# Optimization experiments

Measured on AMD Instinct MI355X. Metric: run time of the kernel, lower is better.

The kernel has to match this reference:

```python
import jax, jax.numpy as jnp
import numpy as np

HQ, HKV, D, RD = 32, 8, 128, 64   # q heads, kv heads, head_dim, rotary_dim
EPS = 1e-6


def _rms_norm(x, w, eps):
    # per-head RMSNorm over last dim (non-gemma: scale by w)
    var = jnp.mean(x * x, axis=-1, keepdims=True)
    return x * jax.lax.rsqrt(var + eps) * w


def _partial_rope(x, c, s, rd):
    # x: [T, H, D]; c/s: [T, rd//2]; NeoX half-split rotation on first rd dims
    x1 = x[..., : rd // 2]
    x2 = x[..., rd // 2 : rd]
    c = c[:, None, :]
    s = s[:, None, :]
    return jnp.concatenate([x1 * c - x2 * s, x2 * c + x1 * s, x[..., rd:]], axis=-1)


def setup_inputs() -> dict:
    key = jax.random.key(0)
    ks = jax.random.split(key, 6)
    B, QL, HID, CACHE = 4, 512, 4096, 512
    T = B * QL
    MAXPOS = 4096
    NPAGES, PS, MP = 256, 16, 64  # total pages, page_size, max pages per seq

    hidden_states = jax.random.normal(ks[0], (T, HID), jnp.float32)
    inv = 1.0 / (10000.0 ** (np.arange(0, RD, 2, dtype=np.float64) / RD))
    ang = np.arange(MAXPOS)[:, None] * inv[None, :]
    cos = jnp.asarray(np.cos(ang), jnp.float32)   # [MAXPOS, RD//2]
    sin = jnp.asarray(np.sin(ang), jnp.float32)
    positions = jnp.tile(CACHE + jnp.arange(QL, dtype=jnp.int32), B)  # [T]
    k_cache = jax.random.normal(ks[1], (NPAGES, PS, HKV, D), jnp.float32)
    v_cache = jax.random.normal(ks[2], (NPAGES, PS, HKV, D), jnp.float32)
    page_table = jnp.arange(B * MP, dtype=jnp.int32).reshape(B, MP)
    cache_seqlens = jnp.full((B,), CACHE, jnp.int32)
    cu_seqlens_q = jnp.arange(B + 1, dtype=jnp.int32) * QL
    qkv_weight = jax.random.normal(ks[3], ((HQ + 2 * HKV) * D, HID), jnp.float32) * 0.02
    o_proj_weight = jax.random.normal(ks[4], (HID, HQ * D), jnp.float32) * 0.02
    q_norm_weight = jnp.ones((D,), jnp.float32)
    k_norm_weight = jnp.ones((D,), jnp.float32)
    return dict(hidden_states=hidden_states, cos=cos, sin=sin, positions=positions,
                k_cache=k_cache, v_cache=v_cache, page_table=page_table,
                cache_seqlens=cache_seqlens, cu_seqlens_q=cu_seqlens_q,
                qkv_weight=qkv_weight, o_proj_weight=o_proj_weight,
                q_norm_weight=q_norm_weight, k_norm_weight=k_norm_weight)


def reference(hidden_states, cos, sin, positions, k_cache, v_cache, page_table,
              cache_seqlens, cu_seqlens_q, qkv_weight, o_proj_weight,
              q_norm_weight, k_norm_weight):
    T = hidden_states.shape[0]
    B = cache_seqlens.shape[0]
    QL = T // B                       # equal-length sequences (extend mode)
    PS = k_cache.shape[1]

    # QKV projection + split
    qkv = hidden_states @ qkv_weight.T
    q, k, v = jnp.split(qkv, [HQ * D, (HQ + HKV) * D], axis=-1)

    # per-head QK RMSNorm (q_norm_weight.shape[0] == head_dim branch)
    q = _rms_norm(q.reshape(T, HQ, D), q_norm_weight, EPS)
    k = _rms_norm(k.reshape(T, HKV, D), k_norm_weight, EPS)
    v = v.reshape(T, HKV, D)

    # partial RoPE
    pc, psn = cos[positions], sin[positions]
    q = _partial_rope(q, pc, psn, RD)
    k = _partial_rope(k, pc, psn, RD)

    # paged KV-cache write: absolute slot = cache_seqlens[b] + j
    pos_abs = cache_seqlens[:, None] + jnp.arange(QL, dtype=jnp.int32)[None, :]  # [B,QL]
    pages = jnp.take_along_axis(page_table, pos_abs // PS, axis=1)
    slots = pos_abs % PS
    k_cache = k_cache.at[pages, slots].set(k.reshape(B, QL, HKV, D))
    v_cache = v_cache.at[pages, slots].set(v.reshape(B, QL, HKV, D))

    # gather per-sequence KV from pages: [B, KV, HKV, D]
    KV = page_table.shape[1] * PS
    keys = k_cache[page_table].reshape(B, KV, HKV, D)
    vals = v_cache[page_table].reshape(B, KV, HKV, D)

    # GQA paged attention with causal mask on absolute positions
    G = HQ // HKV
    qh = q.reshape(B, QL, HKV, G, D)
    scale = 1.0 / np.sqrt(D).astype(np.float32)
    scores = jnp.einsum('bqhgd,bkhd->bhgqk', qh, keys) * scale
    kpos = jnp.arange(KV, dtype=jnp.int32)
    mask = kpos[None, None, :] <= pos_abs[:, :, None]                  # [B,QL,KV]
    scores = jnp.where(mask[:, None, None, :, :], scores, -1e30)
    probs = jax.nn.softmax(scores, axis=-1)
    attn = jnp.einsum('bhgqk,bkhd->bqhgd', probs, vals).reshape(T, HQ * D)

    return attn @ o_proj_weight.T
```

## Files before the change

### kernel.cpp

```cpp
#include <hip/hip_runtime.h>

typedef unsigned int   u32;
typedef unsigned short u16;

typedef float  f32x4  __attribute__((ext_vector_type(4)));
typedef u32    u32x4  __attribute__((ext_vector_type(4)));
typedef u16    u16x4  __attribute__((ext_vector_type(4)));
typedef __bf16 bf16x8 __attribute__((ext_vector_type(8)));

union FragU { u16 us[8]; u32x4 q; bf16x8 v; };

__device__ __forceinline__ u32 f2u(float x){ union{float f;u32 u;}c; c.f=x; return c.u; }
__device__ __forceinline__ float u2f(u32 u){ union{float f;u32 u;}c; c.u=u; return c.f; }
__device__ __forceinline__ u16 bfhi(float x){ u32 u=f2u(x); return (u16)((u + 0x7fffu + ((u>>16)&1u))>>16); }
__device__ __forceinline__ u32 cvtpk(float a, float b){
  u32 r;
  asm("v_cvt_pk_bf16_f32 %0, %1, %2" : "=v"(r) : "v"(a), "v"(b));
  return r;
}

__device__ __forceinline__ void gload16(const void* g, void* l){
  __builtin_amdgcn_global_load_lds(
      (const __attribute__((address_space(1))) unsigned int*)g,
      (__attribute__((address_space(3))) unsigned int*)l, 16, 0, 0);
}

__global__ __launch_bounds__(256)
void prep_pack(const float* __restrict__ s0, u32* __restrict__ d0,
               const float* __restrict__ s1, u32* __restrict__ d1,
               const float* __restrict__ s2, u32* __restrict__ d2)
{
  const int bid = blockIdx.x;
  const float* s; u32* d; int base;
  if (bid < 256)       { s = s0; d = d0; base = bid*4096; }
  else if (bid < 1024) { s = s1; d = d1; base = (bid-256)*4096; }
  else                 { s = s2; d = d2; base = (bid-1024)*4096; }
  int j = base + threadIdx.x;
  #pragma unroll
  for (int it=0; it<8; ++it){
    const int j2 = j + 256;
    f32x4 a0 = __builtin_nontemporal_load(reinterpret_cast<const f32x4*>(s) + 2*j);
    f32x4 a1 = __builtin_nontemporal_load(reinterpret_cast<const f32x4*>(s) + 2*j + 1);
    f32x4 b0 = __builtin_nontemporal_load(reinterpret_cast<const f32x4*>(s) + 2*j2);
    f32x4 b1 = __builtin_nontemporal_load(reinterpret_cast<const f32x4*>(s) + 2*j2 + 1);
    reinterpret_cast<u32x4*>(d)[j] =
      (u32x4){ cvtpk(a0.x,a0.y), cvtpk(a0.z,a0.w), cvtpk(a1.x,a1.y), cvtpk(a1.z,a1.w) };
    reinterpret_cast<u32x4*>(d)[j2] =
      (u32x4){ cvtpk(b0.x,b0.y), cvtpk(b0.z,b0.w), cvtpk(b1.x,b1.y), cvtpk(b1.z,b1.w) };
    j += 512;
  }
}

__global__ __launch_bounds__(256, 2)
void gemm_pkA2(const u16* __restrict__ A, const u16* __restrict__ B,
               float* __restrict__ C, int M, int N, int K)
{
  extern __shared__ char smem[];
  const int tid  = threadIdx.x;
  const int lane = tid & 63;
  const int w    = tid >> 6;
  const int wm = w >> 1, wn = w & 1;
  const int ln = lane & 15, lg = lane >> 4;

  const int nbm = M >> 7;
  const int nbn = N / 192;
  const int nwg = nbm * nbn;
  const int swz = (blockIdx.x & 7) * (nwg >> 3) + (blockIdx.x >> 3);
  const int bm = swz % nbm, bn = swz / nbm;

  const size_t rb = (size_t)K * 2;
  const int lrow  = lane >> 3;
  const int lslot = (lane & 7) ^ (lrow & 7);
  const char* As0 = (const char*)A + (size_t)(bm*128 + w*8 + lrow)*rb + lslot*16;
  const char* Bs0 = (const char*)B + (size_t)(bn*192 + w*8 + lrow)*rb + lslot*16;

  auto stA = [&](int buf, int t) {
    const char* s = As0 + ((size_t)t << 7);
    char* d = smem + buf*40960 + w*1024;
    gload16(s,           d);
    gload16(s +  32*rb,  d + 4096);
    gload16(s +  64*rb,  d + 8192);
    gload16(s +  96*rb,  d + 12288);
  };
  auto stB = [&](int buf, int t) {
    const char* s = Bs0 + ((size_t)t << 7);
    char* d = smem + buf*40960 + 16384 + w*1024;
    gload16(s,           d);
    gload16(s +  32*rb,  d + 4096);
    gload16(s +  64*rb,  d + 8192);
    gload16(s +  96*rb,  d + 12288);
    gload16(s + 128*rb,  d + 16384);
    gload16(s + 160*rb,  d + 20480);
  };

  f32x4 z = {0.f,0.f,0.f,0.f};
  f32x4 acc[4][6];
  #pragma unroll
  for (int i=0;i<4;i++){
    #pragma unroll
    for (int j=0;j<6;j++) acc[i][j] = z;
  }

  const int nt = K >> 6;
  stA(0, 0); stB(0, 0);
  if (nt > 1) { stB(1, 1);
    asm volatile("s_waitcnt vmcnt(6)" ::: "memory");
  } else {
    asm volatile("s_waitcnt vmcnt(0)" ::: "memory");
  }
  __builtin_amdgcn_s_barrier();
  asm volatile("" ::: "memory");

  const int lx7 = ln & 7;

  for (int t = 0; t < nt; ++t){
    const int cur = t & 1;
    const char* bufc = smem + cur*40960;

    FragU bfr[6][2];
    #pragma unroll
    for (int ni=0; ni<6; ni++){
      const int rofs = 16384 + (wn*96 + ni*16 + ln)*128;
      #pragma unroll
      for (int ks=0; ks<2; ks++)
        bfr[ni][ks].q = *reinterpret_cast<const u32x4*>(bufc + rofs + (((ks*4+lg)^lx7)<<4));
    }
    FragU af[2][2];
    #pragma unroll
    for (int mf=0; mf<2; mf++){
      const int rofs = (wm*64 + mf*16 + ln)*128;
      #pragma unroll
      for (int ks=0; ks<2; ks++)
        af[mf][ks].q = *reinterpret_cast<const u32x4*>(bufc + rofs + (((ks*4+lg)^lx7)<<4));
    }
    if (t+1 < nt) stA(cur^1, t+1);
    __builtin_amdgcn_s_barrier();
    __builtin_amdgcn_s_setprio(1);
    #pragma unroll
    for (int ks=0; ks<2; ks++){
      #pragma unroll
      for (int mf=0; mf<2; mf++){
        #pragma unroll
        for (int ni=0; ni<6; ni++)
          acc[mf][ni] = __builtin_amdgcn_mfma_f32_16x16x32_bf16(af[mf][ks].v, bfr[ni][ks].v, acc[mf][ni], 0,0,0);
      }
    }
    __builtin_amdgcn_s_setprio(0);
    asm volatile("s_waitcnt lgkmcnt(0)" ::: "memory");
    __builtin_amdgcn_s_barrier();

    FragU ag[2][2];
    #pragma unroll
    for (int mf=0; mf<2; mf++){
      const int rofs = (wm*64 + (mf+2)*16 + ln)*128;
      #pragma unroll
      for (int ks=0; ks<2; ks++)
        ag[mf][ks].q = *reinterpret_cast<const u32x4*>(bufc + rofs + (((ks*4+lg)^lx7)<<4));
    }
    if (t+2 < nt) stB(cur, t+2);
    __builtin_amdgcn_s_barrier();
    __builtin_amdgcn_s_setprio(1);
    #pragma unroll
    for (int ks=0; ks<2; ks++){
      #pragma unroll
      for (int mf=0; mf<2; mf++){
        #pragma unroll
        for (int ni=0; ni<6; ni++)
          acc[mf+2][ni] = __builtin_amdgcn_mfma_f32_16x16x32_bf16(ag[mf][ks].v, bfr[ni][ks].v, acc[mf+2][ni], 0,0,0);
      }
    }
    __builtin_amdgcn_s_setprio(0);
    if (t+1 < nt){
      if (t+2 < nt) asm volatile("s_waitcnt vmcnt(6)" ::: "memory");
      else          asm volatile("s_waitcnt vmcnt(0)" ::: "memory");
    }
    __builtin_amdgcn_s_barrier();
    asm volatile("" ::: "memory");
  }

  #pragma unroll
  for (int mi=0; mi<4; mi++){
    #pragma unroll
    for (int ni=0; ni<6; ni++){
      const int row0 = bm*128 + wm*64 + mi*16 + lg*4;
      const int col  = bn*192 + wn*96 + ni*16 + ln;
      #pragma unroll
      for (int r=0; r<4; r++)
        C[(size_t)(row0+r)*N + col] = acc[mi][ni][r];
    }
  }
}

__global__ __launch_bounds__(256, 2)
void gemm_pkB2(const u16* __restrict__ A, const u16* __restrict__ B,
               float* __restrict__ C, int M, int N, int K)
{
  extern __shared__ char smem[];
  const int tid  = threadIdx.x;
  const int lane = tid & 63;
  const int w    = tid >> 6;
  const int wm = w >> 1, wn = w & 1;
  const int ln = lane & 15, lg = lane >> 4;

  const int nbm = M >> 7, nbn = N >> 7;
  const int nwg = nbm * nbn;
  const int swz = (blockIdx.x & 7) * (nwg >> 3) + (blockIdx.x >> 3);
  const int bm = swz % nbm, bn = swz / nbm;

  const size_t rb = (size_t)K * 2;
  const int lrow  = lane >> 3;
  const int lslot = (lane & 7) ^ (lrow & 7);
  const char* As0 = (const char*)A + (size_t)(bm*128 + w*8 + lrow)*rb + lslot*16;
  const char* Bs0 = (const char*)B + (size_t)(bn*128 + w*8 + lrow)*rb + lslot*16;

  auto stA = [&](int buf, int t) {
    const char* s = As0 + ((size_t)t << 7);
    char* d = smem + buf*32768 + w*1024;
    gload16(s,           d);
    gload16(s +  32*rb,  d + 4096);
    gload16(s +  64*rb,  d + 8192);
    gload16(s +  96*rb,  d + 12288);
  };
  auto stB = [&](int buf, int t) {
    const char* s = Bs0 + ((size_t)t << 7);
    char* d = smem + buf*32768 + 16384 + w*1024;
    gload16(s,           d);
    gload16(s +  32*rb,  d + 4096);
    gload16(s +  64*rb,  d + 8192);
    gload16(s +  96*rb,  d + 12288);
  };

  f32x4 z = {0.f,0.f,0.f,0.f};
  f32x4 acc[4][4];
  #pragma unroll
  for (int i=0;i<4;i++){
    #pragma unroll
    for (int j=0;j<4;j++) acc[i][j] = z;
  }

  const int nt = K >> 6;
  stA(0, 0); stB(0, 0);
  if (nt > 1) { stB(1, 1);
    asm volatile("s_waitcnt vmcnt(4)" ::: "memory");
  } else {
    asm volatile("s_waitcnt vmcnt(0)" ::: "memory");
  }
  __builtin_amdgcn_s_barrier();
  asm volatile("" ::: "memory");

  const int lx7 = ln & 7;

  for (int t = 0; t < nt; ++t){
    const int cur = t & 1;
    const char* bufc = smem + cur*32768;

    FragU bfr[4][2];
    #pragma unroll
    for (int ni=0; ni<4; ni++){
      const int rofs = 16384 + (wn*64 + ni*16 + ln)*128;
      #pragma unroll
      for (int ks=0; ks<2; ks++)
        bfr[ni][ks].q = *reinterpret_cast<const u32x4*>(bufc + rofs + (((ks*4+lg)^lx7)<<4));
    }
    FragU af[2][2];
    #pragma unroll
    for (int mf=0; mf<2; mf++){
      const int rofs = (wm*64 + mf*16 + ln)*128;
      #pragma unroll
      for (int ks=0; ks<2; ks++)
        af[mf][ks].q = *reinterpret_cast<const u32x4*>(bufc + rofs + (((ks*4+lg)^lx7)<<4));
    }
    if (t+1 < nt) stA(cur^1, t+1);
    __builtin_amdgcn_s_barrier();
    __builtin_amdgcn_s_setprio(1);
    #pragma unroll
    for (int ks=0; ks<2; ks++){
      #pragma unroll
      for (int mf=0; mf<2; mf++){
        #pragma unroll
        for (int ni=0; ni<4; ni++)
          acc[mf][ni] = __builtin_amdgcn_mfma_f32_16x16x32_bf16(af[mf][ks].v, bfr[ni][ks].v, acc[mf][ni], 0,0,0);
      }
    }
    __builtin_amdgcn_s_setprio(0);
    asm volatile("s_waitcnt lgkmcnt(0)" ::: "memory");
    __builtin_amdgcn_s_barrier();

    FragU ag[2][2];
    #pragma unroll
    for (int mf=0; mf<2; mf++){
      const int rofs = (wm*64 + (mf+2)*16 + ln)*128;
      #pragma unroll
      for (int ks=0; ks<2; ks++)
        ag[mf][ks].q = *reinterpret_cast<const u32x4*>(bufc + rofs + (((ks*4+lg)^lx7)<<4));
    }
    if (t+2 < nt) stB(cur, t+2);
    __builtin_amdgcn_s_barrier();
    __builtin_amdgcn_s_setprio(1);
    #pragma unroll
    for (int ks=0; ks<2; ks++){
      #pragma unroll
      for (int mf=0; mf<2; mf++){
        #pragma unroll
        for (int ni=0; ni<4; ni++)
          acc[mf+2][ni] = __builtin_amdgcn_mfma_f32_16x16x32_bf16(ag[mf][ks].v, bfr[ni][ks].v, acc[mf+2][ni], 0,0,0);
      }
    }
    __builtin_amdgcn_s_setprio(0);
    if (t+1 < nt){
      if (t+2 < nt) asm volatile("s_waitcnt vmcnt(4)" ::: "memory");
      else          asm volatile("s_waitcnt vmcnt(0)" ::: "memory");
    }
    __builtin_amdgcn_s_barrier();
    asm volatile("" ::: "memory");
  }

  #pragma unroll
  for (int mi=0; mi<4; mi++){
    #pragma unroll
    for (int ni=0; ni<4; ni++){
      const int row0 = bm*128 + wm*64 + mi*16 + lg*4;
      const int col  = bn*128 + wn*64 + ni*16 + ln;
      #pragma unroll
      for (int r=0; r<4; r++)
        C[(size_t)(row0+r)*N + col] = acc[mi][ni][r];
    }
  }
}

__global__ __launch_bounds__(256)
void norm_gather_kv(const float* __restrict__ qkv, const float* __restrict__ cosT,
                    const float* __restrict__ sinT, const int* __restrict__ positions,
                    const int* __restrict__ cache_seqlens,
                    const float* __restrict__ kw,
                    const float* __restrict__ k_cache, const float* __restrict__ v_cache,
                    const int* __restrict__ page_table,
                    u16* __restrict__ k_all, u16* __restrict__ v_allT)
{
  const int tid = threadIdx.x;
  if (blockIdx.x < 2048){
    const int t = blockIdx.x;
    const int lane = tid & 63;
    const int w = tid >> 6;
    const int b = t >> 9;
    const int q = t & 511;
    const int pos  = positions[t];
    const int cpos = cache_seqlens[b] + q;
    for (int it=0; it<4; ++it){
      int hh = it*4 + w;
      const float* xp = qkv + (size_t)t*6144 + (32+hh)*128 + 2*lane;
      float2 x = *reinterpret_cast<const float2*>(xp);
      if (hh < 8){
        float ss = x.x*x.x + x.y*x.y;
        #pragma unroll
        for (int mk=1; mk<64; mk<<=1) ss += __shfl_xor(ss, mk);
        float var = ss*(1.0f/128.0f) + 1e-6f;
        float rq = rsqrtf(var);
        rq = rq*(1.5f - 0.5f*var*rq*rq);
        x.x *= rq*kw[2*lane]; x.y *= rq*kw[2*lane+1];
        float px = __shfl_xor(x.x, 16);
        float py = __shfl_xor(x.y, 16);
        if (lane < 32){
          int ci = pos*32 + 2*(lane&15);
          float2 cc = *reinterpret_cast<const float2*>(cosT + ci);
          float2 sc = *reinterpret_cast<const float2*>(sinT + ci);
          if (lane < 16){ x.x = x.x*cc.x - px*sc.x; x.y = x.y*cc.y - py*sc.y; }
          else          { x.x = x.x*cc.x + px*sc.x; x.y = x.y*cc.y + py*sc.y; }
        }
        u16* kp = k_all + ((size_t)(b*8 + hh)*1024 + cpos)*128 + 2*lane;
        kp[0] = bfhi(x.x); kp[1] = bfhi(x.y);
      } else {
        u16* vp = v_allT + ((size_t)(b*8 + (hh-8))*128 + 2*lane)*1024 + cpos;
        vp[0]    = bfhi(x.x);
        vp[1024] = bfhi(x.y);
      }
    }
    return;
  }
  __shared__ float tb[32][129];
  const int id = blockIdx.x - 2048;
  const int jt = id & 31, h = (id>>5)&7, b = id>>8;
  const int j0 = jt*32;
  const int csb = cache_seqlens[b];
  if (j0 >= csb) return;
  {
    int r = tid>>3, c = tid&7;
    int j = j0 + r;
    int page = page_table[b*64 + (j>>4)];
    int slot = j & 15;
    const float* ks = k_cache + (size_t)((page*16 + slot)*8 + h)*128;
    const float* vs = v_cache + (size_t)((page*16 + slot)*8 + h)*128;
    u16* kd = k_all + ((size_t)(b*8+h)*1024 + j)*128;
    const bool wr = (j < csb);
    #pragma unroll
    for (int i=0;i<2;i++){
      int d0i = (c + 8*i)*8;
      f32x4 ka = __builtin_nontemporal_load(reinterpret_cast<const f32x4*>(ks + d0i));
      f32x4 kb = __builtin_nontemporal_load(reinterpret_cast<const f32x4*>(ks + d0i + 4));
      if (wr)
        *reinterpret_cast<u32x4*>(kd + d0i) =
          (u32x4){ cvtpk(ka.x,ka.y), cvtpk(ka.z,ka.w), cvtpk(kb.x,kb.y), cvtpk(kb.z,kb.w) };
      f32x4 va = __builtin_nontemporal_load(reinterpret_cast<const f32x4*>(vs + d0i));
      f32x4 vb = __builtin_nontemporal_load(reinterpret_cast<const f32x4*>(vs + d0i + 4));
      tb[r][d0i+0]=va.x; tb[r][d0i+1]=va.y; tb[r][d0i+2]=va.z; tb[r][d0i+3]=va.w;
      tb[r][d0i+4]=vb.x; tb[r][d0i+5]=vb.y; tb[r][d0i+6]=vb.z; tb[r][d0i+7]=vb.w;
    }
  }
  __syncthreads();
  {
    int dout = tid>>1, jh = tid&1;
    u16* vd = v_allT + ((size_t)(b*8+h)*128 + dout)*1024 + j0 + jh*16;
    #pragma unroll
    for (int i=0;i<2;i++){
      if (j0 + jh*16 + i*8 < csb){
        int jb = jh*16 + i*8;
        u32x4 o = { cvtpk(tb[jb+0][dout], tb[jb+1][dout]),
                    cvtpk(tb[jb+2][dout], tb[jb+3][dout]),
                    cvtpk(tb[jb+4][dout], tb[jb+5][dout]),
                    cvtpk(tb[jb+6][dout], tb[jb+7][dout]) };
        *reinterpret_cast<u32x4*>(vd + i*8) = o;
      }
    }
  }
}

__global__ __launch_bounds__(512)
void attn_fused9(const float* __restrict__ qkv, const float* __restrict__ cosT,
                 const float* __restrict__ sinT, const int* __restrict__ positions,
                 const float* __restrict__ qw,
                 const u16* __restrict__ k_all, const u16* __restrict__ v_allT,
                 const int* __restrict__ cache_seqlens, u16* __restrict__ attnO)
{
  extern __shared__ char smem[];
  const int tid = threadIdx.x, lane = tid&63, w = tid>>6;
  const int ln = lane&15, lg = lane>>4;
  const int id = blockIdx.x;
  const int qt = id & 3, g = (id>>2)&3, kvh = (id>>4)&7, b = id>>7;
  const int cs = cache_seqlens[b];
  const int h  = kvh*4 + g;
  const int q0 = qt*128 + w*16;
  const float SCALE = 0.08838834764831845f;
  f32x4 z = {0.f,0.f,0.f,0.f};

  FragU qf[4];
  {
    const int row = b*512 + q0 + ln;
    const float* qp = qkv + (size_t)row*6144 + h*128;
    float xq[4][8];
    float ss = 0.f;
    #pragma unroll
    for (int ks=0; ks<4; ks++){
      int d0 = ks*32 + lg*8;
      f32x4 a = *reinterpret_cast<const f32x4*>(qp + d0);
      f32x4 c = *reinterpret_cast<const f32x4*>(qp + d0 + 4);
      xq[ks][0]=a.x; xq[ks][1]=a.y; xq[ks][2]=a.z; xq[ks][3]=a.w;
      xq[ks][4]=c.x; xq[ks][5]=c.y; xq[ks][6]=c.z; xq[ks][7]=c.w;
      #pragma unroll
      for (int k2=0;k2<8;k2++) ss += xq[ks][k2]*xq[ks][k2];
    }
    ss += __shfl_xor(ss, 16);
    ss += __shfl_xor(ss, 32);
    float var = ss*(1.0f/128.0f) + 1e-6f;
    float rq = rsqrtf(var);
    rq = rq*(1.5f - 0.5f*var*rq*rq);
    rq *= SCALE;
    #pragma unroll
    for (int ks=0; ks<4; ks++){
      int d0 = ks*32 + lg*8;
      f32x4 wa = *reinterpret_cast<const f32x4*>(qw + d0);
      f32x4 wb = *reinterpret_cast<const f32x4*>(qw + d0 + 4);
      xq[ks][0]*=rq*wa.x; xq[ks][1]*=rq*wa.y; xq[ks][2]*=rq*wa.z; xq[ks][3]*=rq*wa.w;
      xq[ks][4]*=rq*wb.x; xq[ks][5]*=rq*wb.y; xq[ks][6]*=rq*wb.z; xq[ks][7]*=rq*wb.w;
    }
    const int pos = positions[row];
    const int ci = pos*32 + lg*8;
    #pragma unroll
    for (int k2=0;k2<8;k2+=4){
      f32x4 cc = *reinterpret_cast<const f32x4*>(cosT + ci + k2);
      f32x4 sc = *reinterpret_cast<const f32x4*>(sinT + ci + k2);
      float cA[4] = {cc.x,cc.y,cc.z,cc.w};
      float sA[4] = {sc.x,sc.y,sc.z,sc.w};
      #pragma unroll
      for (int u=0;u<4;u++){
        float x1 = xq[0][k2+u], x2 = xq[1][k2+u];
        xq[0][k2+u] = x1*cA[u] - x2*sA[u];
        xq[1][k2+u] = x2*cA[u] + x1*sA[u];
      }
    }
    #pragma unroll
    for (int ks=0; ks<4; ks++)
      qf[ks].q = (u32x4){ cvtpk(xq[ks][0],xq[ks][1]), cvtpk(xq[ks][2],xq[ks][3]),
                          cvtpk(xq[ks][4],xq[ks][5]), cvtpk(xq[ks][6],xq[ks][7]) };
  }

  f32x4 O[8];
  #pragma unroll
  for (int i=0;i<8;i++) O[i] = z;
  float lacc[4] = {0.f,0.f,0.f,0.f};
  const int prow0 = cs + q0 + lg*4;
  const int nt = (cs + qt*128 + 128 + 63) >> 6;
  const char* kbase = (const char*)(k_all  + (size_t)(b*8+kvh)*1024*128);
  const char* vbase = (const char*)(v_allT + (size_t)(b*8+kvh)*128*1024);

  auto stK = [&](int buf, int t){
    #pragma unroll
    for (int i=0;i<2;i++){
      int row = i*32 + w*4 + (lane>>4);
      const char* s = kbase + (size_t)(t*64 + row)*256 + (((lane&15) ^ (row&7))<<4);
      gload16(s, smem + buf*16384 + i*8192 + w*1024);
    }
  };
  auto stV = [&](int buf, int t){
    #pragma unroll
    for (int i=0;i<2;i++){
      int row = i*64 + w*8 + (lane>>3);
      const char* s = vbase + (size_t)row*2048 + (size_t)t*128 + (((lane&7) ^ (row&7))<<4);
      gload16(s, smem + 32768 + buf*16384 + i*8192 + w*1024);
    }
  };

  stK(0, 0); stV(0, 0);
  if (nt > 1){ stK(1, 1); stV(1, 1); }

  for (int tile=0; tile<nt; ++tile){
    const int cur = tile & 1;
    const int kv0 = tile*64;
    if (tile+1 < nt) asm volatile("s_waitcnt vmcnt(4)" ::: "memory");
    else             asm volatile("s_waitcnt vmcnt(0)" ::: "memory");
    __builtin_amdgcn_s_barrier();

    const u16* Kc = (const u16*)(smem + cur*16384);
    f32x4 s[4]; s[0]=z; s[1]=z; s[2]=z; s[3]=z;
    #pragma unroll
    for (int ks=0; ks<4; ks++){
      int so = ((ks*4+lg) ^ (ln&7)) << 3;
      #pragma unroll
      for (int n=0; n<4; n++){
        FragU kf;
        kf.q = *reinterpret_cast<const u32x4*>(&Kc[(n*16+ln)*128 + so]);
        s[n] = __builtin_amdgcn_mfma_f32_16x16x32_bf16(qf[ks].v, kf.v, s[n], 0,0,0);
      }
    }

    float pv[4][4];
    if (kv0 + 63 <= cs + q0){
      #pragma unroll
      for (int n=0;n<4;n++){
        #pragma unroll
        for (int r=0;r<4;r++) pv[n][r] = __expf(s[n][r]);
      }
    } else {
      #pragma unroll
      for (int n=0;n<4;n++){
        #pragma unroll
        for (int r=0;r<4;r++){
          bool ok = (kv0 + n*16 + ln) <= (prow0 + r);
          pv[n][r] = ok ? __expf(s[n][r]) : 0.f;
        }
      }
    }
    #pragma unroll
    for (int r=0;r<4;r++) lacc[r] += (pv[0][r] + pv[1][r]) + (pv[2][r] + pv[3][r]);

    #pragma unroll
    for (int n=0;n<4;n++){
      #pragma unroll
      for (int rp=0; rp<2; rp++){
        u32 hpk = cvtpk(pv[n][rp*2], pv[n][rp*2+1]);
        int col  = n*16 + ln;
        int row0 = lg*4 + rp*2;
        int b0 = w*2048 + row0*128 + ((((col>>3) ^ ((row0>>1)&7)))<<4) + (col&7)*2;
        *(u16*)(smem + 65536 + b0)       = (u16)hpk;
        *(u16*)(smem + 65536 + b0 + 128) = (u16)(hpk >> 16);
      }
    }
    FragU pa[2];
    #pragma unroll
    for (int ks2=0; ks2<2; ks2++)
      pa[ks2].q = *reinterpret_cast<const u32x4*>(
          smem + 65536 + w*2048 + ln*128 + (((ks2*4+lg) ^ ((ln>>1)&7))<<4));

    const char* Vb = smem + 32768 + cur*16384;
    #pragma unroll
    for (int nf=0; nf<8; nf++){
      int dr = nf*16 + ln;
      #pragma unroll
      for (int ks2=0; ks2<2; ks2++){
        FragU vf;
        vf.q = *reinterpret_cast<const u32x4*>(Vb + dr*128 + (((ks2*4+lg) ^ (dr&7))<<4));
        O[nf] = __builtin_amdgcn_mfma_f32_16x16x32_bf16(pa[ks2].v, vf.v, O[nf], 0,0,0);
      }
    }
    asm volatile("s_waitcnt lgkmcnt(0)" ::: "memory");
    __builtin_amdgcn_s_barrier();
    if (tile+2 < nt){ stK(cur, tile+2); stV(cur, tile+2); }
  }

  #pragma unroll
  for (int off=1; off<16; off<<=1){
    #pragma unroll
    for (int r=0;r<4;r++) lacc[r] += __shfl_xor(lacc[r], off);
  }
  float il[4];
  #pragma unroll
  for (int r=0;r<4;r++) il[r] = 1.0f / lacc[r];
  u16* op = attnO + (size_t)(b*512 + q0 + lg*4)*4096 + h*128 + ln;
  #pragma unroll
  for (int nf=0; nf<8; nf++){
    #pragma unroll
    for (int r=0;r<4;r++)
      op[(size_t)r*4096 + nf*16] = bfhi(O[nf][r] * il[r]);
  }
}

extern "C" void kernel_launch(void* const* d_in, const int* in_sizes, int n_in,
                              void* d_out, int out_size, void* d_ws, size_t ws_size,
                              hipStream_t stream) {
  const float* hidden    = (const float*)d_in[0];
  const float* cosT      = (const float*)d_in[1];
  const float* sinT      = (const float*)d_in[2];
  const int*   positions = (const int*)  d_in[3];
  const float* k_cache   = (const float*)d_in[4];
  const float* v_cache   = (const float*)d_in[5];
  const int*   page_tab  = (const int*)  d_in[6];
  const int*   cache_sl  = (const int*)  d_in[7];
  const float* qkv_w     = (const float*)d_in[9];
  const float* o_w       = (const float*)d_in[10];
  const float* qnw       = (const float*)d_in[11];
  const float* knw       = (const float*)d_in[12];
  float* out = (float*)d_out;

  float* qkv   = (float*)d_ws;
  u16* k_all   = (u16*)(qkv + 12582912);
  u16* v_allT  = k_all  + 4194304;
  u16* attnPk  = v_allT + 4194304;
  u16* hidPk   = attnPk + 8388608;
  u16* qkvwPk  = hidPk  + 8388608;
  u16* owPk    = qkvwPk + 25165824;
  (void)in_sizes; (void)n_in; (void)out_size; (void)ws_size;

  (void)hipFuncSetAttribute(reinterpret_cast<const void*>(gemm_pkA2),
                            hipFuncAttributeMaxDynamicSharedMemorySize, 81920);
  (void)hipFuncSetAttribute(reinterpret_cast<const void*>(gemm_pkB2),
                            hipFuncAttributeMaxDynamicSharedMemorySize, 65536);
  (void)hipFuncSetAttribute(reinterpret_cast<const void*>(attn_fused9),
                            hipFuncAttributeMaxDynamicSharedMemorySize, 81920);

  hipLaunchKernelGGL(prep_pack, dim3(1536), dim3(256), 0, stream,
                     hidden, (u32*)hidPk,
                     qkv_w, (u32*)qkvwPk,
                     o_w, (u32*)owPk);
  hipLaunchKernelGGL(gemm_pkA2, dim3(512), dim3(256), 81920, stream,
                     hidPk, qkvwPk, qkv, 2048, 6144, 4096);
  hipLaunchKernelGGL(norm_gather_kv, dim3(3072), dim3(256), 0, stream,
                     qkv, cosT, sinT, positions, cache_sl, knw,
                     k_cache, v_cache, page_tab, k_all, v_allT);
  hipLaunchKernelGGL(attn_fused9, dim3(512), dim3(512), 81920, stream,
                     qkv, cosT, sinT, positions, qnw, k_all, v_allT, cache_sl, attnPk);
  hipLaunchKernelGGL(gemm_pkB2, dim3(512), dim3(256), 65536, stream,
                     attnPk, owPk, out, 2048, 4096, 4096);
}
```

Baseline: 294.4 us.

## Split GEMM K-step into four phases interleaving A/B global loads with MFMA

Restructures the main GEMM loop from two compute phases into four, each loading one 16-row A fragment and issuing a slice of the next-tile global-to-LDS loads between barriers. It spreads the A and B prefetches across the iteration so memory traffic overlaps more evenly with MFMA work, and it keeps fewer A fragment registers live. In exchange it adds two more barriers per K-step and depends on the existing vmcnt accounting still matching the reordered loads.

```diff
diff --git a/kernel.cpp b/kernel.cpp
--- a/kernel.cpp
+++ b/kernel.cpp
@@ -116,6 +116,12 @@
   for (int t = 0; t < nt; ++t){
     const int cur = t & 1;
     const char* bufc = smem + cur*40960;
+    const bool hasA = (t+1 < nt);
+    const bool hasB = (t+2 < nt);
+    const char* sA1 = As0 + ((size_t)(t+1) << 7);
+    char*       dA1 = smem + (cur^1)*40960 + w*1024;
+    const char* sB2 = Bs0 + ((size_t)(t+2) << 7);
+    char*       dB2 = smem + cur*40960 + 16384 + w*1024;
 
     FragU bfr[6][2];
     #pragma unroll
@@ -125,54 +131,89 @@
       for (int ks=0; ks<2; ks++)
         bfr[ni][ks].q = *reinterpret_cast<const u32x4*>(bufc + rofs + (((ks*4+lg)^lx7)<<4));
     }
-    FragU af[2][2];
-    #pragma unroll
-    for (int mf=0; mf<2; mf++){
-      const int rofs = (wm*64 + mf*16 + ln)*128;
+    FragU af[2];
+    {
+      const int rofs = (wm*64 + ln)*128;
       #pragma unroll
       for (int ks=0; ks<2; ks++)
-        af[mf][ks].q = *reinterpret_cast<const u32x4*>(bufc + rofs + (((ks*4+lg)^lx7)<<4));
-    }
-    if (t+1 < nt) stA(cur^1, t+1);
+        af[ks].q = *reinterpret_cast<const u32x4*>(bufc + rofs + (((ks*4+lg)^lx7)<<4));
+    }
+    if (hasA){ gload16(sA1, dA1); gload16(sA1 + 32*rb, dA1 + 4096); }
     __builtin_amdgcn_s_barrier();
     __builtin_amdgcn_s_setprio(1);
     #pragma unroll
     for (int ks=0; ks<2; ks++){
       #pragma unroll
-      for (int mf=0; mf<2; mf++){
-        #pragma unroll
-        for (int ni=0; ni<6; ni++)
-          acc[mf][ni] = __builtin_amdgcn_mfma_f32_16x16x32_bf16(af[mf][ks].v, bfr[ni][ks].v, acc[mf][ni], 0,0,0);
-      }
+      for (int ni=0; ni<6; ni++)
+        acc[0][ni] = __builtin_amdgcn_mfma_f32_16x16x32_bf16(af[ks].v, bfr[ni][ks].v, acc[0][ni], 0,0,0);
     }
     __builtin_amdgcn_s_setprio(0);
     asm volatile("s_waitcnt lgkmcnt(0)" ::: "memory");
     __builtin_amdgcn_s_barrier();
 
-    FragU ag[2][2];
-    #pragma unroll
-    for (int mf=0; mf<2; mf++){
-      const int rofs = (wm*64 + (mf+2)*16 + ln)*128;
+    {
+      const int rofs = (wm*64 + 16 + ln)*128;
       #pragma unroll
       for (int ks=0; ks<2; ks++)
-        ag[mf][ks].q = *reinterpret_cast<const u32x4*>(bufc + rofs + (((ks*4+lg)^lx7)<<4));
-    }
-    if (t+2 < nt) stB(cur, t+2);
+        af[ks].q = *reinterpret_cast<const u32x4*>(bufc + rofs + (((ks*4+lg)^lx7)<<4));
+    }
+    if (hasA){ gload16(sA1 + 64*rb, dA1 + 8192); gload16(sA1 + 96*rb, dA1 + 12288); }
     __builtin_amdgcn_s_barrier();
     __builtin_amdgcn_s_setprio(1);
     #pragma unroll
     for (int ks=0; ks<2; ks++){
       #pragma unroll
-      for (int mf=0; mf<2; mf++){
-        #pragma unroll
-        for (int ni=0; ni<6; ni++)
-          acc[mf+2][ni] = __builtin_amdgcn_mfma_f32_16x16x32_bf16(ag[mf][ks].v, bfr[ni][ks].v, acc[mf+2][ni], 0,0,0);
-      }
+      for (int ni=0; ni<6; ni++)
+        acc[1][ni] = __builtin_amdgcn_mfma_f32_16x16x32_bf16(af[ks].v, bfr[ni][ks].v, acc[1][ni], 0,0,0);
     }
     __builtin_amdgcn_s_setprio(0);
-    if (t+1 < nt){
-      if (t+2 < nt) asm volatile("s_waitcnt vmcnt(6)" ::: "memory");
-      else          asm volatile("s_waitcnt vmcnt(0)" ::: "memory");
+    __builtin_amdgcn_s_barrier();
+
+    {
+      const int rofs = (wm*64 + 32 + ln)*128;
+      #pragma unroll
+      for (int ks=0; ks<2; ks++)
+        af[ks].q = *reinterpret_cast<const u32x4*>(bufc + rofs + (((ks*4+lg)^lx7)<<4));
+    }
+    if (hasB){
+      gload16(sB2,           dB2);
+      gload16(sB2 +  32*rb,  dB2 + 4096);
+      gload16(sB2 +  64*rb,  dB2 + 8192);
+    }
+    __builtin_amdgcn_s_barrier();
+    __builtin_amdgcn_s_setprio(1);
+    #pragma unroll
+    for (int ks=0; ks<2; ks++){
+      #pragma unroll
+      for (int ni=0; ni<6; ni++)
+        acc[2][ni] = __builtin_amdgcn_mfma_f32_16x16x32_bf16(af[ks].v, bfr[ni][ks].v, acc[2][ni], 0,0,0);
+    }
+    __builtin_amdgcn_s_setprio(0);
+    __builtin_amdgcn_s_barrier();
+
+    {
+      const int rofs = (wm*64 + 48 + ln)*128;
+      #pragma unroll
+      for (int ks=0; ks<2; ks++)
+        af[ks].q = *reinterpret_cast<const u32x4*>(bufc + rofs + (((ks*4+lg)^lx7)<<4));
+    }
+    if (hasB){
+      gload16(sB2 +  96*rb,  dB2 + 12288);
+      gload16(sB2 + 128*rb,  dB2 + 16384);
+      gload16(sB2 + 160*rb,  dB2 + 20480);
+    }
+    __builtin_amdgcn_s_barrier();
+    __builtin_amdgcn_s_setprio(1);
+    #pragma unroll
+    for (int ks=0; ks<2; ks++){
+      #pragma unroll
+      for (int ni=0; ni<6; ni++)
+        acc[3][ni] = __builtin_amdgcn_mfma_f32_16x16x32_bf16(af[ks].v, bfr[ni][ks].v, acc[3][ni], 0,0,0);
+    }
+    __builtin_amdgcn_s_setprio(0);
+    if (hasA){
+      if (hasB) asm volatile("s_waitcnt vmcnt(6)" ::: "memory");
+      else      asm volatile("s_waitcnt vmcnt(0)" ::: "memory");
     }
     __builtin_amdgcn_s_barrier();
     asm volatile("" ::: "memory");
```

After: 292.5 us. Within noise of the previous version (-0.6%).
